# Optimization experiments

Hardware: AMD Instinct MI355X
Metric: run time of the kernel (lower is better)

Reference implementation:

```python
import jax, jax.numpy as jnp
import numpy as np

N = 100000      # nodes
EG = 600000     # global (knn) edges used by GAT layers
E = 600000      # prediction edges scored by edge_mlp
H = 1           # gat_heads
C = 64          # hidden_dim (per-head out channels)
HC = H * C
EDGE_IN = 2 * HC + 2  # 130
EDGE_HID = EDGE_IN * 4  # 520


def gat_layer(x, W, att_src, att_dst, bias, src, dst):
    # PyG GATConv (concat=True, residual=False, no edge_dim, eval mode)
    n = x.shape[0]
    h = (x @ W).reshape(n, H, C)                      # [N,H,C]
    a_s = jnp.sum(h * att_src, axis=-1)               # [N,H]
    a_d = jnp.sum(h * att_dst, axis=-1)               # [N,H]
    alpha = jax.nn.leaky_relu(a_s[src] + a_d[dst], 0.2)  # [Eg,H]
    amax = jax.ops.segment_max(alpha, dst, num_segments=n)
    amax = jnp.where(jnp.isfinite(amax), amax, 0.0)
    e = jnp.exp(alpha - amax[dst])
    denom = jax.ops.segment_sum(e, dst, num_segments=n)
    w = e / (denom[dst] + 1e-16)                      # scatter-softmax over in-edges of dst
    out = jax.ops.segment_sum(h[src] * w[:, :, None], dst, num_segments=n)
    return out.reshape(n, HC) + bias


def setup_inputs() -> dict:
    key = jax.random.key(0)
    ks = jax.random.split(key, 16)
    glorot = lambda k, shape: jax.random.normal(k, shape, jnp.float32) * np.sqrt(2.0 / (shape[0] + shape[-1]))
    inp = {
        "pos": jax.random.normal(ks[0], (N, 3), jnp.float32),
        "edge_index": jax.random.randint(ks[1], (2, E), 0, N, jnp.int32),
        "global_edge_index": jax.random.randint(ks[2], (2, EG), 0, N, jnp.int32),
        "edge_attr": jax.random.uniform(ks[3], (E, 2), jnp.float32),
        # GAT layer 0 (in=3)
        "W0": glorot(ks[4], (3, HC)),
        "att_src0": glorot(ks[5], (1, H, C)),
        "att_dst0": glorot(ks[6], (1, H, C)),
        "b0": jnp.zeros((HC,), jnp.float32),
        # GAT layer 1 (in=HC)
        "W1": glorot(ks[7], (HC, HC)),
        "att_src1": glorot(ks[8], (1, H, C)),
        "att_dst1": glorot(ks[9], (1, H, C)),
        "b1": jnp.zeros((HC,), jnp.float32),
        # edge MLP: Linear(130,520) -> ELU -> Linear(520,1)
        "Wm1": glorot(ks[10], (EDGE_IN, EDGE_HID)),
        "bm1": jnp.zeros((EDGE_HID,), jnp.float32),
        "Wm2": glorot(ks[11], (EDGE_HID, 1)),
        "bm2": jnp.zeros((1,), jnp.float32),
    }
    return inp


def reference(pos, edge_index, global_edge_index, edge_attr,
              W0, att_src0, att_dst0, b0,
              W1, att_src1, att_dst1, b1,
              Wm1, bm1, Wm2, bm2):
    gsrc, gdst = global_edge_index[0], global_edge_index[1]
    x = pos  # dropout p=0 -> identity
    x = jax.nn.elu(gat_layer(x, W0, att_src0, att_dst0, b0, gsrc, gdst))
    x = jax.nn.elu(gat_layer(x, W1, att_src1, att_dst1, b1, gsrc, gdst))
    # per-edge gather-concat-MLP
    esrc, edst = edge_index[0], edge_index[1]
    ef = jnp.concatenate([x[esrc], x[edst], edge_attr], axis=1)  # [E, 130]
    h = jax.nn.elu(ef @ Wm1 + bm1)
    edge_values = (h @ Wm2 + bm2)[:, 0]  # [E]
    return edge_values
```

## Files before the change

kernel.cpp:

```cpp
#include <hip/hip_runtime.h>

#define KN 100000
#define KEG 600000
#define KE 600000
#define NB 98
#define LOG2E 1.4426950408889634f
#define LN2 0.6931471805599453f

#define FB_PREP 391
#define FB_CVEC 33
#define FB_HIST 2344
#define FB_T0 25000

using u16 = unsigned short;
typedef __bf16 bf16x8 __attribute__((ext_vector_type(8)));
typedef float f32x4 __attribute__((ext_vector_type(4)));

__device__ __forceinline__ float b2f(u16 u) { return __uint_as_float(((unsigned)u) << 16); }
__device__ __forceinline__ u16 f2b(float f) {
  unsigned u = __float_as_uint(f);
  u += 0x7FFF + ((u >> 16) & 1);
  return (u16)(u >> 16);
}
__device__ __forceinline__ int imin(int a, int b) { return a < b ? a : b; }
__device__ __forceinline__ float fexp2(float x) {
#if __has_builtin(__builtin_amdgcn_exp2f)
  return __builtin_amdgcn_exp2f(x);
#else
  return __expf(x * LN2);
#endif
}

__global__ __launch_bounds__(256) void k_front(
    const float* __restrict__ pos, const float* __restrict__ W0,
    const float* __restrict__ att_s, const float* __restrict__ att_d,
    const float* __restrict__ wm1, const float* __restrict__ bm1,
    const float* __restrict__ wm2, const float* __restrict__ w1,
    const int* __restrict__ gdst,
    u16* __restrict__ wm1t, u16* __restrict__ w1t, float2* __restrict__ wsc2,
    float* __restrict__ w2sum, int* __restrict__ counts,
    u16* __restrict__ h, float* __restrict__ a_s, float* __restrict__ a_d) {
  int bid = blockIdx.x;
  if (bid < FB_PREP) {
    int idx = bid * 256 + threadIdx.x;
    if (idx < 33 * 5 * 512) {
      int j = idx & 7;
      int lane = (idx >> 3) & 63;
      int f = (idx >> 9) % 5;
      int nt = idx / (512 * 5);
      int n = nt * 16 + (lane & 15);
      float v = 0.f;
      if (n < 520) {
        if (f < 4) {
          int k = f * 32 + (lane >> 4) * 8 + j;
          v = wm1[k * 520 + n] * LOG2E;
        } else {
          int kk = (lane >> 4) * 8 + j;
          if (kk == 0) v = wm1[128 * 520 + n] * LOG2E;
          else if (kk == 1) v = wm1[129 * 520 + n] * LOG2E;
          else if (kk == 2) v = bm1[n] * LOG2E;
        }
      }
      wm1t[idx] = f2b(v);
    }
    if (idx < 33 * 64) {
      int lane = idx & 63, nt = idx >> 6;
      int col = nt * 16 + (lane & 15);
      float w2 = (col < 520) ? wm2[col] : 0.f;
      float2 p; p.x = w2; p.y = -LN2 * w2;
      wsc2[idx] = p;
    }
    if (idx < 4 * 2 * 64 * 8) {
      int j = idx & 7;
      int lane = (idx >> 3) & 63;
      int kt = (idx >> 9) & 1;
      int nt = idx >> 10;
      int n = nt * 16 + (lane & 15);
      int k = kt * 32 + (lane >> 4) * 8 + j;
      w1t[idx] = f2b(w1[k * 64 + n]);
    }
  } else if (bid < FB_PREP + FB_CVEC) {
    int lane = threadIdx.x & 63;
    int w = (bid - FB_PREP) * 4 + (threadIdx.x >> 6);
    float x = 0.f;
    if (w <= 129) {
      const float* row = wm1 + (size_t)w * 520;
#pragma unroll
      for (int j = 0; j < 8; ++j) x += row[j * 64 + lane] * wm2[j * 64 + lane];
      if (lane < 8) x += row[512 + lane] * wm2[512 + lane];
    } else if (w == 130) {
#pragma unroll
      for (int j = 0; j < 8; ++j) x += bm1[j * 64 + lane] * wm2[j * 64 + lane];
      if (lane < 8) x += bm1[512 + lane] * wm2[512 + lane];
    } else if (w == 131) {
#pragma unroll
      for (int j = 0; j < 8; ++j) x += wm2[j * 64 + lane];
      if (lane < 8) x += wm2[512 + lane];
    }
    for (int off = 1; off < 64; off <<= 1) x += __shfl_xor(x, off);
    if (w <= 130 && lane < 16) {
      int f = w >> 5, kk = w & 31;
      int qq = kk >> 3, jj = kk & 7;
      u16 chi = f2b(x);
      float v = (lane == 0) ? x : (lane == 1 ? (x - b2f(chi)) : 0.f);
      wm1t[(33 * 5 + f) * 512 + (qq * 16 + lane) * 8 + jj] = f2b(v);
    } else if (w == 131 && lane == 0) {
      w2sum[0] = x;
    }
  } else if (bid < FB_PREP + FB_CVEC + FB_HIST) {
    int e = (bid - (FB_PREP + FB_CVEC)) * 256 + threadIdx.x;
    if (e < KEG) atomicAdd(counts + gdst[e], 1);
  } else {
    int lane = threadIdx.x & 63;
    int n = (bid - (FB_PREP + FB_CVEC + FB_HIST)) * 4 + (threadIdx.x >> 6);
    float p0 = pos[n * 3 + 0], p1 = pos[n * 3 + 1], p2 = pos[n * 3 + 2];
    float hv = p0 * W0[lane] + p1 * W0[64 + lane] + p2 * W0[128 + lane];
    h[n * 64 + lane] = f2b(hv);
    float s = hv * att_s[lane];
    float d = hv * att_d[lane];
    for (int off = 1; off < 64; off <<= 1) { s += __shfl_xor(s, off); d += __shfl_xor(d, off); }
    if (lane == 0) { a_s[n] = s; a_d[n] = d; }
  }
}


__global__ __launch_bounds__(1024) void k_scan_block(
    const int* __restrict__ counts, int* __restrict__ incl, int* __restrict__ bsum) {
  int gid = blockIdx.x * 1024 + threadIdx.x;
  int lane = threadIdx.x & 63, w = threadIdx.x >> 6;
  int x = (gid < KN) ? counts[gid] : 0;
  for (int off = 1; off < 64; off <<= 1) {
    int y = __shfl_up(x, off);
    if (lane >= off) x += y;
  }
  __shared__ int wtot[16];
  if (lane == 63) wtot[w] = x;
  __syncthreads();
  if (w == 0 && lane < 16) {
    int t = wtot[lane];
    for (int off = 1; off < 16; off <<= 1) {
      int y = __shfl_up(t, off);
      if (lane >= off) t += y;
    }
    wtot[lane] = t;
  }
  __syncthreads();
  if (w > 0) x += wtot[w - 1];
  if (gid < KN) incl[gid] = x;
  if (threadIdx.x == 1023) bsum[blockIdx.x] = x;
}

__global__ __launch_bounds__(64) void k_scan_bsum(const int* __restrict__ bsum, int* __restrict__ boff) {
  int lane = threadIdx.x;
  int x0 = (lane < NB) ? bsum[lane] : 0;
  int x1 = (64 + lane < NB) ? bsum[64 + lane] : 0;
  int i0 = x0, i1 = x1;
  for (int off = 1; off < 64; off <<= 1) {
    int y0 = __shfl_up(i0, off), y1 = __shfl_up(i1, off);
    if (lane >= off) { i0 += y0; i1 += y1; }
  }
  int tot0 = __shfl(i0, 63);
  if (lane < NB) boff[lane] = i0 - x0;
  if (64 + lane < NB) boff[64 + lane] = i1 - x1 + tot0;
}

__global__ __launch_bounds__(1024) void k_scan_final(
    const int* __restrict__ incl, const int* __restrict__ counts,
    const int* __restrict__ boff, int* __restrict__ row_start) {
  int gid = blockIdx.x * 1024 + threadIdx.x;
  if (gid < KN) row_start[gid] = incl[gid] - counts[gid] + boff[blockIdx.x];
}

__global__ __launch_bounds__(256) void k_fill(
    const int* __restrict__ gsrc, const int* __restrict__ gdst,
    const int* __restrict__ row_start, int* __restrict__ cursor,
    const float* __restrict__ a_s, const float* __restrict__ a_d,
    int* __restrict__ csr_src, int* __restrict__ csr_dst, float* __restrict__ ew) {
  int e = blockIdx.x * 256 + threadIdx.x;
  if (e >= KEG) return;
  int s = gsrc[e], d = gdst[e];
  int pos = atomicAdd(cursor + d, 1);
  int slot = row_start[d] + pos;
  csr_src[slot] = s;
  csr_dst[slot] = d;
  float al = a_s[s] + a_d[d];
  al = al > 0.f ? al : 0.2f * al;
  ew[slot] = __expf(al);
}

__global__ __launch_bounds__(256) void k_ew(
    const int* __restrict__ csr_src, const int* __restrict__ csr_dst,
    const float* __restrict__ a_s, const float* __restrict__ a_d, float* __restrict__ ew) {
  int slot = blockIdx.x * 256 + threadIdx.x;
  if (slot >= KEG) return;
  float al = a_s[csr_src[slot]] + a_d[csr_dst[slot]];
  al = al > 0.f ? al : 0.2f * al;
  ew[slot] = __expf(al);
}


__global__ __launch_bounds__(256) void k_transform1(
    const u16* __restrict__ x, const u16* __restrict__ w1t,
    const float* __restrict__ att_s, const float* __restrict__ att_d,
    u16* __restrict__ h, float* __restrict__ a_s, float* __restrict__ a_d) {
  int lane = threadIdx.x & 63;
  int wave = threadIdx.x >> 6;
  int nodebase = blockIdx.x * 64 + wave * 16;
  int m = lane & 15, q = lane >> 4;

  int node = imin(nodebase + m, KN - 1);
  const bf16x8* px = (const bf16x8*)(x + node * 64);
  bf16x8 A0 = px[q];
  bf16x8 A1 = px[q + 4];

  const bf16x8* bt = (const bf16x8*)w1t;
  float ps[4] = {0.f, 0.f, 0.f, 0.f};
  float pd[4] = {0.f, 0.f, 0.f, 0.f};
#pragma unroll
  for (int nt = 0; nt < 4; ++nt) {
    int col = nt * 16 + m;
    float asv = att_s[col], adv = att_d[col];
    f32x4 acc = {0.f, 0.f, 0.f, 0.f};
    acc = __builtin_amdgcn_mfma_f32_16x16x32_bf16(A0, bt[(nt * 2 + 0) * 64 + lane], acc, 0, 0, 0);
    acc = __builtin_amdgcn_mfma_f32_16x16x32_bf16(A1, bt[(nt * 2 + 1) * 64 + lane], acc, 0, 0, 0);
#pragma unroll
    for (int r = 0; r < 4; ++r) {
      int rown = nodebase + q * 4 + r;
      if (rown < KN) h[rown * 64 + col] = f2b(acc[r]);
      ps[r] += acc[r] * asv;
      pd[r] += acc[r] * adv;
    }
  }
#pragma unroll
  for (int r = 0; r < 4; ++r) {
    float s = ps[r], d = pd[r];
    s += __shfl_xor(s, 1); d += __shfl_xor(d, 1);
    s += __shfl_xor(s, 2); d += __shfl_xor(d, 2);
    s += __shfl_xor(s, 4); d += __shfl_xor(d, 4);
    s += __shfl_xor(s, 8); d += __shfl_xor(d, 8);
    int rown = nodebase + q * 4 + r;
    if (m == 0 && rown < KN) { a_s[rown] = s; a_d[rown] = d; }
  }
}

__global__ __launch_bounds__(256) void k_gat_agg(
    const int* __restrict__ row_start, const int* __restrict__ counts,
    const int* __restrict__ csr_src, const float* __restrict__ ew,
    const u16* __restrict__ h, const float* __restrict__ bias, u16* __restrict__ xout) {
  int lane = threadIdx.x & 63;
  int n = blockIdx.x * 4 + (threadIdx.x >> 6);
  int start = row_start[n], deg = counts[n];
  float acc = 0.f, den = 0.f;
  int j = 0;
  for (; j + 4 <= deg; j += 4) {
    int s0 = csr_src[start + j];
    int s1 = csr_src[start + j + 1];
    int s2 = csr_src[start + j + 2];
    int s3 = csr_src[start + j + 3];
    float w0 = ew[start + j], w1 = ew[start + j + 1];
    float w2 = ew[start + j + 2], w3 = ew[start + j + 3];
    float h0 = b2f(h[s0 * 64 + lane]);
    float h1 = b2f(h[s1 * 64 + lane]);
    float h2 = b2f(h[s2 * 64 + lane]);
    float h3 = b2f(h[s3 * 64 + lane]);
    den += (w0 + w1) + (w2 + w3);
    acc += w0 * h0 + w1 * h1 + w2 * h2 + w3 * h3;
  }
  for (; j < deg; ++j) {
    int s0 = csr_src[start + j];
    float w0 = ew[start + j];
    den += w0;
    acc += w0 * b2f(h[s0 * 64 + lane]);
  }
  float v = acc / (den + 1e-16f) + bias[lane];
  v = v > 0.f ? v : expm1f(v);
  xout[n * 64 + lane] = f2b(v);
}

__global__ __launch_bounds__(256) void k_edge_mlp(
    const int* __restrict__ eidx, const u16* __restrict__ x2bf,
    const float* __restrict__ eattr, const u16* __restrict__ wm1t,
    const float2* __restrict__ wsc2, const float* __restrict__ w2sum,
    const float* __restrict__ bm2, float* __restrict__ out) {
  int lane = threadIdx.x & 63;
  int wave = threadIdx.x >> 6;
  int base = blockIdx.x * 256 + wave * 64;
  int m = lane & 15, q = lane >> 4;

  bf16x8 A[4][4];
#pragma unroll
  for (int s = 0; s < 4; ++s) {
    int row = imin(base + s * 16 + m, KE - 1);
    int es = eidx[row], ed = eidx[KE + row];
    const bf16x8* psrc = (const bf16x8*)(x2bf + es * 64);
    const bf16x8* pdst = (const bf16x8*)(x2bf + ed * 64);
    A[s][0] = psrc[q];
    A[s][1] = psrc[q + 4];
    A[s][2] = pdst[q];
    A[s][3] = pdst[q + 4];
  }
  bf16x8 A5[4];
#pragma unroll
  for (int s = 0; s < 4; ++s) {
    bf16x8 a5 = {0, 0, 0, 0, 0, 0, 0, 0};
    if (q == 0) {
      int row = imin(base + s * 16 + m, KE - 1);
      a5[0] = (__bf16)eattr[row * 2 + 0];
      a5[1] = (__bf16)eattr[row * 2 + 1];
      a5[2] = (__bf16)1.0f;
    }
    A5[s] = a5;
  }

  float osum[4][4];
#pragma unroll
  for (int s = 0; s < 4; ++s)
#pragma unroll
    for (int r = 0; r < 4; ++r) osum[s][r] = 0.f;

  const bf16x8* bt = (const bf16x8*)wm1t;
  int phase = (wave * 8 + (blockIdx.x & 7)) % 33;
#pragma unroll 1
  for (int i = 0; i < 33; ++i) {
    int nt = i + phase;
    if (nt >= 33) nt -= 33;
    bf16x8 B0 = bt[(nt * 5 + 0) * 64 + lane];
    bf16x8 B1 = bt[(nt * 5 + 1) * 64 + lane];
    bf16x8 B2 = bt[(nt * 5 + 2) * 64 + lane];
    bf16x8 B3 = bt[(nt * 5 + 3) * 64 + lane];
    bf16x8 B4 = bt[(nt * 5 + 4) * 64 + lane];
    float2 w2 = wsc2[nt * 64 + lane];
#pragma unroll
    for (int s = 0; s < 4; ++s) {
      f32x4 acc = {0.f, 0.f, 0.f, 0.f};
      acc = __builtin_amdgcn_mfma_f32_16x16x32_bf16(A[s][0], B0, acc, 0, 0, 0);
      acc = __builtin_amdgcn_mfma_f32_16x16x32_bf16(A[s][1], B1, acc, 0, 0, 0);
      acc = __builtin_amdgcn_mfma_f32_16x16x32_bf16(A[s][2], B2, acc, 0, 0, 0);
      acc = __builtin_amdgcn_mfma_f32_16x16x32_bf16(A[s][3], B3, acc, 0, 0, 0);
      acc = __builtin_amdgcn_mfma_f32_16x16x32_bf16(A5[s],   B4, acc, 0, 0, 0);
#pragma unroll
      for (int r = 0; r < 4; ++r) {
        float tt = fminf(acc[r], 0.f);
        float e = fexp2(tt);
        osum[s][r] += e * w2.x;
        osum[s][r] += tt * w2.y;
      }
    }
  }

  bf16x8 L0 = bt[(33 * 5 + 0) * 64 + lane];
  bf16x8 L1 = bt[(33 * 5 + 1) * 64 + lane];
  bf16x8 L2 = bt[(33 * 5 + 2) * 64 + lane];
  bf16x8 L3 = bt[(33 * 5 + 3) * 64 + lane];
  bf16x8 L4 = bt[(33 * 5 + 4) * 64 + lane];
  float w2s = w2sum[0];
  float b2v = bm2[0];

#pragma unroll
  for (int s = 0; s < 4; ++s) {
    f32x4 accL = {0.f, 0.f, 0.f, 0.f};
    accL = __builtin_amdgcn_mfma_f32_16x16x32_bf16(A[s][0], L0, accL, 0, 0, 0);
    accL = __builtin_amdgcn_mfma_f32_16x16x32_bf16(A[s][1], L1, accL, 0, 0, 0);
    accL = __builtin_amdgcn_mfma_f32_16x16x32_bf16(A[s][2], L2, accL, 0, 0, 0);
    accL = __builtin_amdgcn_mfma_f32_16x16x32_bf16(A[s][3], L3, accL, 0, 0, 0);
    accL = __builtin_amdgcn_mfma_f32_16x16x32_bf16(A5[s],   L4, accL, 0, 0, 0);
#pragma unroll
    for (int r = 0; r < 4; ++r) {
      float lin = accL[r] + __shfl_xor(accL[r], 1);
      float v = osum[s][r];
      v += __shfl_xor(v, 1);
      v += __shfl_xor(v, 2);
      v += __shfl_xor(v, 4);
      v += __shfl_xor(v, 8);
      if (m == 0) {
        int row = base + s * 16 + q * 4 + r;
        if (row < KE) out[row] = v - w2s + lin + b2v;
      }
    }
  }
}

extern "C" void kernel_launch(void* const* d_in, const int* in_sizes, int n_in,
                              void* d_out, int out_size, void* d_ws, size_t ws_size,
                              hipStream_t stream) {
  const float* pos  = (const float*)d_in[0];
  const int* eidx   = (const int*)d_in[1];
  const int* geidx  = (const int*)d_in[2];
  const float* eattr= (const float*)d_in[3];
  const float* W0   = (const float*)d_in[4];
  const float* as0  = (const float*)d_in[5];
  const float* ad0  = (const float*)d_in[6];
  const float* b0   = (const float*)d_in[7];
  const float* W1   = (const float*)d_in[8];
  const float* as1  = (const float*)d_in[9];
  const float* ad1  = (const float*)d_in[10];
  const float* b1   = (const float*)d_in[11];
  const float* Wm1  = (const float*)d_in[12];
  const float* bm1  = (const float*)d_in[13];
  const float* Wm2  = (const float*)d_in[14];
  const float* bm2  = (const float*)d_in[15];
  float* out = (float*)d_out;

  char* ws = (char*)d_ws;
  size_t off = 0;
  auto carve = [&](size_t bytes) {
    char* p = ws + off;
    off = (off + bytes + 255) & ~(size_t)255;
    return p;
  };
  int* counts    = (int*)carve((size_t)KN * 4);
  int* cursor    = (int*)carve((size_t)KN * 4);
  int* incl      = (int*)carve((size_t)KN * 4);
  int* row_start = (int*)carve((size_t)KN * 4);
  int* bsum      = (int*)carve(128 * 4);
  int* boff      = (int*)carve(128 * 4);
  int* csr_src   = (int*)carve((size_t)KEG * 4);
  int* csr_dst   = (int*)carve((size_t)KEG * 4);
  float* ew      = (float*)carve((size_t)KEG * 4);
  u16* h         = (u16*)carve((size_t)KN * 64 * 2);
  u16* x12       = (u16*)carve((size_t)KN * 64 * 2);
  float* a_s     = (float*)carve((size_t)KN * 4);
  float* a_d     = (float*)carve((size_t)KN * 4);
  u16* wm1t      = (u16*)carve((size_t)34 * 5 * 512 * 2);
  u16* w1t       = (u16*)carve((size_t)4 * 2 * 64 * 8 * 2);
  float2* wsc2   = (float2*)carve((size_t)33 * 64 * 8);
  float* w2sum   = (float*)carve(256);

  const int* gsrc = geidx;
  const int* gdst = geidx + KEG;

  hipMemsetAsync(d_ws, 0, 800128, stream);

  k_front<<<FB_PREP + FB_CVEC + FB_HIST + FB_T0, 256, 0, stream>>>(
      pos, W0, as0, ad0, Wm1, bm1, Wm2, W1, gdst,
      wm1t, w1t, wsc2, w2sum, counts, h, a_s, a_d);

  k_scan_block<<<NB, 1024, 0, stream>>>(counts, incl, bsum);
  k_scan_bsum<<<1, 64, 0, stream>>>(bsum, boff);
  k_scan_final<<<NB, 1024, 0, stream>>>(incl, counts, boff, row_start);
  k_fill<<<(KEG + 255) / 256, 256, 0, stream>>>(gsrc, gdst, row_start, cursor,
                                                a_s, a_d, csr_src, csr_dst, ew);

  k_gat_agg<<<KN / 4, 256, 0, stream>>>(row_start, counts, csr_src, ew, h, b0, x12);

  k_transform1<<<(KN + 63) / 64, 256, 0, stream>>>(x12, w1t, as1, ad1, h, a_s, a_d);
  k_ew<<<(KEG + 255) / 256, 256, 0, stream>>>(csr_src, csr_dst, a_s, a_d, ew);
  k_gat_agg<<<KN / 4, 256, 0, stream>>>(row_start, counts, csr_src, ew, h, b1, x12);

  k_edge_mlp<<<(KE + 255) / 256, 256, 0, stream>>>(eidx, x12, eattr, wm1t, wsc2, w2sum, bm2, out);
}
```

Baseline: 408.4 us.

## Stage edge-MLP weight tiles through double-buffered LDS and pack epilogue math

Inside the edge-MLP kernel, the 33 weight tiles are no longer read directly from global memory by every wave. Each block now cooperatively loads each tile into a double-buffered shared-memory slot, prefetching the next tile while the current one feeds the MFMAs. The per-tile accumulation is also rewritten as packed two-wide float ops. This cuts redundant global/L2 weight traffic, but adds a block barrier per tile and drops the per-wave phase staggering.

```diff
diff --git a/kernel.cpp b/kernel.cpp
--- a/kernel.cpp
+++ b/kernel.cpp
@@ -15,6 +15,7 @@
 using u16 = unsigned short;
 typedef __bf16 bf16x8 __attribute__((ext_vector_type(8)));
 typedef float f32x4 __attribute__((ext_vector_type(4)));
+typedef float f32x2 __attribute__((ext_vector_type(2)));
 
 __device__ __forceinline__ float b2f(u16 u) { return __uint_as_float(((unsigned)u) << 16); }
 __device__ __forceinline__ u16 f2b(float f) {
@@ -282,6 +283,7 @@
     const float* __restrict__ eattr, const u16* __restrict__ wm1t,
     const float2* __restrict__ wsc2, const float* __restrict__ w2sum,
     const float* __restrict__ bm2, float* __restrict__ out) {
+  __shared__ uint4 Bbuf[2][5 * 64];
   int lane = threadIdx.x & 63;
   int wave = threadIdx.x >> 6;
   int base = blockIdx.x * 256 + wave * 64;
@@ -312,24 +314,39 @@
     A5[s] = a5;
   }
 
-  float osum[4][4];
-#pragma unroll
-  for (int s = 0; s < 4; ++s)
-#pragma unroll
-    for (int r = 0; r < 4; ++r) osum[s][r] = 0.f;
-
-  const bf16x8* bt = (const bf16x8*)wm1t;
-  int phase = (wave * 8 + (blockIdx.x & 7)) % 33;
+  f32x2 osum[4][2];
+#pragma unroll
+  for (int s = 0; s < 4; ++s) {
+    osum[s][0] = (f32x2){0.f, 0.f};
+    osum[s][1] = (f32x2){0.f, 0.f};
+  }
+
+  const uint4* gB = (const uint4*)wm1t;
+  {
+    uint4 s0 = gB[(0 * 5 + wave) * 64 + lane];
+    Bbuf[0][wave * 64 + lane] = s0;
+    if (wave == 0) {
+      uint4 s1 = gB[(0 * 5 + 4) * 64 + lane];
+      Bbuf[0][4 * 64 + lane] = s1;
+    }
+  }
+  __syncthreads();
+
 #pragma unroll 1
-  for (int i = 0; i < 33; ++i) {
-    int nt = i + phase;
-    if (nt >= 33) nt -= 33;
-    bf16x8 B0 = bt[(nt * 5 + 0) * 64 + lane];
-    bf16x8 B1 = bt[(nt * 5 + 1) * 64 + lane];
-    bf16x8 B2 = bt[(nt * 5 + 2) * 64 + lane];
-    bf16x8 B3 = bt[(nt * 5 + 3) * 64 + lane];
-    bf16x8 B4 = bt[(nt * 5 + 4) * 64 + lane];
+  for (int nt = 0; nt < 33; ++nt) {
+    int cur = nt & 1, nxt = cur ^ 1;
+    uint4 st0, st1;
+    if (nt < 32) {
+      st0 = gB[((nt + 1) * 5 + wave) * 64 + lane];
+      if (wave == 0) st1 = gB[((nt + 1) * 5 + 4) * 64 + lane];
+    }
     float2 w2 = wsc2[nt * 64 + lane];
+    const bf16x8* lb = (const bf16x8*)Bbuf[cur];
+    bf16x8 B0 = lb[0 * 64 + lane];
+    bf16x8 B1 = lb[1 * 64 + lane];
+    bf16x8 B2 = lb[2 * 64 + lane];
+    bf16x8 B3 = lb[3 * 64 + lane];
+    bf16x8 B4 = lb[4 * 64 + lane];
 #pragma unroll
     for (int s = 0; s < 4; ++s) {
       f32x4 acc = {0.f, 0.f, 0.f, 0.f};
@@ -338,16 +355,21 @@
       acc = __builtin_amdgcn_mfma_f32_16x16x32_bf16(A[s][2], B2, acc, 0, 0, 0);
       acc = __builtin_amdgcn_mfma_f32_16x16x32_bf16(A[s][3], B3, acc, 0, 0, 0);
       acc = __builtin_amdgcn_mfma_f32_16x16x32_bf16(A5[s],   B4, acc, 0, 0, 0);
-#pragma unroll
-      for (int r = 0; r < 4; ++r) {
-        float tt = fminf(acc[r], 0.f);
-        float e = fexp2(tt);
-        osum[s][r] += e * w2.x;
-        osum[s][r] += tt * w2.y;
-      }
-    }
-  }
-
+      f32x2 t0 = {fminf(acc[0], 0.f), fminf(acc[1], 0.f)};
+      f32x2 t1 = {fminf(acc[2], 0.f), fminf(acc[3], 0.f)};
+      f32x2 e0 = {fexp2(t0.x), fexp2(t0.y)};
+      f32x2 e1 = {fexp2(t1.x), fexp2(t1.y)};
+      osum[s][0] += e0 * w2.x + t0 * w2.y;
+      osum[s][1] += e1 * w2.x + t1 * w2.y;
+    }
+    if (nt < 32) {
+      Bbuf[nxt][wave * 64 + lane] = st0;
+      if (wave == 0) Bbuf[nxt][4 * 64 + lane] = st1;
+    }
+    __syncthreads();
+  }
+
+  const bf16x8* bt = (const bf16x8*)wm1t;
   bf16x8 L0 = bt[(33 * 5 + 0) * 64 + lane];
   bf16x8 L1 = bt[(33 * 5 + 1) * 64 + lane];
   bf16x8 L2 = bt[(33 * 5 + 2) * 64 + lane];
@@ -364,10 +386,11 @@
     accL = __builtin_amdgcn_mfma_f32_16x16x32_bf16(A[s][2], L2, accL, 0, 0, 0);
     accL = __builtin_amdgcn_mfma_f32_16x16x32_bf16(A[s][3], L3, accL, 0, 0, 0);
     accL = __builtin_amdgcn_mfma_f32_16x16x32_bf16(A5[s],   L4, accL, 0, 0, 0);
+    float ov[4] = {osum[s][0].x, osum[s][0].y, osum[s][1].x, osum[s][1].y};
 #pragma unroll
     for (int r = 0; r < 4; ++r) {
       float lin = accL[r] + __shfl_xor(accL[r], 1);
-      float v = osum[s][r];
+      float v = ov[r];
       v += __shfl_xor(v, 1);
       v += __shfl_xor(v, 2);
       v += __shfl_xor(v, 4);
```

Result: no change. 400.6 us (-1.9%).
